# Optimization experiments

Hardware: AMD Instinct MI355X
Metric: run time of the kernel (lower is better)

The kernel has to match this reference:

```python
import jax, jax.numpy as jnp
import numpy as np

HYP_C = 0.1
TAU = 0.1
MRG = 0.1
CLIP_R = 2.3
BS = 1024
NB_PROXIES = 256
SZ_EMBED = 128
T_BATCH = BS * 50
T_LCA = NB_PROXIES * 50


@jax.custom_vjp
def artanh(x):
    xc = jnp.clip(x, -1.0 + 1e-5, 1.0 - 1e-5)
    return 0.5 * (jnp.log1p(xc) - jnp.log1p(-xc))

def _artanh_fwd(x):
    xc = jnp.clip(x, -1.0 + 1e-5, 1.0 - 1e-5)
    return 0.5 * (jnp.log1p(xc) - jnp.log1p(-xc)), xc

def _artanh_bwd(xc, g):
    return (g / (1.0 - xc * xc),)

artanh.defvjp(_artanh_fwd, _artanh_bwd)


@jax.custom_vjp
def riemannian_fix(x):
    # identity fwd; bwd rescales euclidean grad to riemannian grad on the ball
    return x

def _riem_fwd(x):
    return x, x

def _riem_bwd(x, g):
    scale = ((1.0 - HYP_C * jnp.sum(x * x, axis=-1, keepdims=True)) ** 2) / 4.0
    return (g * scale,)

riemannian_fix.defvjp(_riem_fwd, _riem_bwd)


def expmap0(x, c):
    sqrt_c = c ** 0.5
    xn = jnp.maximum(jnp.linalg.norm(x, axis=-1, keepdims=True), 1e-5)
    return jnp.tanh(sqrt_c * xn) * x / (sqrt_c * xn)


def project(x, c):
    norm = jnp.maximum(jnp.linalg.norm(x, axis=-1, keepdims=True), 1e-5)
    maxnorm = (1.0 - 1e-3) / (c ** 0.5)
    return jnp.where(norm > maxnorm, x / norm * maxnorm, x)


def to_poincare(x, c, clip_r):
    xn = jnp.linalg.norm(x, axis=-1, keepdims=True) + 1e-5
    x = x * jnp.minimum(jnp.ones_like(xn), clip_r / xn)
    return riemannian_fix(project(expmap0(x, c), c))


def dist_matrix(x, y, c):
    # ||mobius_add(-x, y)|| computed in closed form (same math as the [N,M,D]
    # num/denom construction in the torch code; num_{nm} = a*( -x_n ) + b*y_m).
    sqrt_c = c ** 0.5
    xy = -jnp.einsum('nd,md->nm', x, y)        # (-x) . y
    x2 = jnp.sum(x * x, axis=-1, keepdims=True)  # [N,1]
    y2t = jnp.sum(y * y, axis=-1)[None, :]       # [1,M]
    a = 1.0 + 2.0 * c * xy + c * y2t             # coeff of -x
    b = 1.0 - c * x2                             # coeff of y
    denom = 1.0 + 2.0 * c * xy + (c ** 2) * x2 * y2t
    num_sq = a * a * x2 + 2.0 * a * b * xy + b * b * y2t
    norm = jnp.sqrt(jnp.maximum(num_sq, 1e-12)) / jnp.abs(denom + 1e-5)
    return (2.0 / sqrt_c) * artanh(sqrt_c * norm)


def gumbel_softmax_hard(logits, g):
    # straight-through hard gumbel softmax (tau=1 as in F.gumbel_softmax default)
    y = jax.nn.softmax(logits + g, axis=-1)
    hard = jax.nn.one_hot(jnp.argmax(y, axis=-1), y.shape[-1], dtype=y.dtype)
    return y + jax.lax.stop_gradient(hard - y)


def compute_ghhc(cp_dist, trip, g):
    i, j, k = trip[0], trip[1], trip[2]
    di, dj, dk = cp_dist[i], cp_dist[j], cp_dist[k]   # [T,P] each
    max_ij = jnp.maximum(di, dj)
    p_ij = gumbel_softmax_hard(-max_ij / TAU, g[0])
    max_ijk = jnp.maximum(dk, max_ij)
    p_ijk = gumbel_softmax_hard(-max_ijk / TAU, g[1])
    diff_lca = (jnp.argmax(p_ij, -1) != jnp.argmax(p_ijk, -1)).astype(cp_dist.dtype)
    d_i_ij = jnp.sum(di * p_ij, axis=1)
    d_i_ijk = jnp.sum(di * p_ijk, axis=1)
    d_j_ij = jnp.sum(dj * p_ij, axis=1)
    d_j_ijk = jnp.sum(dj * p_ijk, axis=1)
    d_k_ij = jnp.sum(dk * p_ij, axis=1)
    d_k_ijk = jnp.sum(dk * p_ijk, axis=1)
    hc = (jax.nn.relu(d_i_ij - d_i_ijk + MRG)
          + jax.nn.relu(d_j_ij - d_j_ijk + MRG)
          + jax.nn.relu(d_k_ijk - d_k_ij + MRG))
    return jnp.mean(hc * diff_lca)


def hp_loss(z_s, t_s, lcas, trip1, trip2, trip3, trip4, g1, g2, g3, g4):
    bs = z_s.shape[0]
    lh = to_poincare(lcas, HYP_C, CLIP_R)
    all_nodes = jnp.concatenate([z_s, lh], axis=0)
    D = dist_matrix(all_nodes, all_nodes, HYP_C)
    t_all = jnp.concatenate([t_s, lh], axis=0)
    Dt = dist_matrix(t_all, t_all, HYP_C)
    loss = compute_ghhc(D[:bs, bs:], trip1, g1)
    loss = loss + compute_ghhc(D[bs:, bs:], trip2, g2)
    loss = loss + compute_ghhc(Dt[:bs, bs:], trip3, g3)
    loss = loss + compute_ghhc(Dt[bs:, bs:], trip4, g4)
    return loss


def setup_inputs() -> dict:
    key = jax.random.key(0)
    ks = jax.random.split(key, 12)
    z_s = jax.random.normal(ks[0], (BS, SZ_EMBED), dtype=jnp.float32)
    t_s = jax.random.normal(ks[1], (BS, SZ_EMBED), dtype=jnp.float32)
    y = jax.random.uniform(ks[2], (BS, 24), dtype=jnp.float32)
    # lcas param init: randn / sqrt(d) * clip_r * 0.9
    lcas = jax.random.normal(ks[3], (NB_PROXIES, SZ_EMBED), dtype=jnp.float32)
    lcas = lcas / np.sqrt(SZ_EMBED) * CLIP_R * 0.9
    trip1 = jax.random.randint(ks[4], (3, T_BATCH), 0, BS, dtype=jnp.int32)
    trip2 = jax.random.randint(ks[5], (3, T_LCA), 0, NB_PROXIES, dtype=jnp.int32)
    trip3 = jax.random.randint(ks[6], (3, T_BATCH), 0, BS, dtype=jnp.int32)
    trip4 = jax.random.randint(ks[7], (3, T_LCA), 0, NB_PROXIES, dtype=jnp.int32)
    g1 = jax.random.gumbel(ks[8], (2, T_BATCH, NB_PROXIES), dtype=jnp.float32)
    g2 = jax.random.gumbel(ks[9], (2, T_LCA, NB_PROXIES), dtype=jnp.float32)
    g3 = jax.random.gumbel(ks[10], (2, T_BATCH, NB_PROXIES), dtype=jnp.float32)
    g4 = jax.random.gumbel(ks[11], (2, T_LCA, NB_PROXIES), dtype=jnp.float32)
    return {"z_s": z_s, "t_s": t_s, "y": y, "lcas": lcas,
            "trip1": trip1, "trip2": trip2, "trip3": trip3, "trip4": trip4,
            "g1": g1, "g2": g2, "g3": g3, "g4": g4}


def reference(z_s, t_s, y, lcas, trip1, trip2, trip3, trip4, g1, g2, g3, g4):
    # y only feeds the detached numpy mining loop in the original; the mined
    # triplets are supplied precomputed (trip1..4), so y does not enter the math.
    return hp_loss(z_s, t_s, lcas, trip1, trip2, trip3, trip4, g1, g2, g3, g4)
```

## Files before the change

kernel.cpp:

```cpp
#include <hip/hip_runtime.h>
#include <cstddef>
#include <stdint.h>

#define HYP_C   0.1f
#define SQRT_C  0.31622776601683794f
#define CLIP_R  2.3f
#define MRG     0.1f
#define NPROX   256
#define DIM     128

#define OFF_LH   0
#define OFF_LHT  32768
#define OFF_LN2  65536
#define OFF_D1   65792
#define OFF_D2   327936
#define OFF_D3   393472

__global__ __launch_bounds__(128)
void to_poincare_kernel(const float* __restrict__ lcas,
                        float* __restrict__ ws,
                        float* __restrict__ out)
{
    const int row = blockIdx.x;
    const int k   = threadIdx.x;
    if (row == 0 && k == 0) out[0] = 0.0f;

    float v  = lcas[row * DIM + k];
    float ss = v * v;
    #pragma unroll
    for (int off = 32; off >= 1; off >>= 1)
        ss += __shfl_xor(ss, off, 64);
    __shared__ float wpart[2];
    if ((k & 63) == 0) wpart[k >> 6] = ss;
    __syncthreads();
    const float sumsq = wpart[0] + wpart[1];

    const float s1 = sqrtf(sumsq);
    const float xn = s1 + 1e-5f;
    const float f1 = fminf(1.0f, CLIP_R / xn);
    const float xn2 = fmaxf(f1 * s1, 1e-5f);
    const float th  = tanhf(SQRT_C * xn2);
    const float f2  = th / (SQRT_C * xn2);
    const float nr      = fmaxf(f2 * f1 * s1, 1e-5f);
    const float maxnorm = (1.0f - 1e-3f) / SQRT_C;
    const float f3      = (nr > maxnorm) ? (maxnorm / nr) : 1.0f;

    const float f  = f3 * f2 * f1;
    const float lv = f * v;
    ws[OFF_LH  + row * DIM + k]   = lv;
    ws[OFF_LHT + k * NPROX + row] = lv;
    if (k == 0) ws[OFF_LN2 + row] = f * f * sumsq;
}

__global__ __launch_bounds__(256)
void dist_all_kernel(const float* __restrict__ z,
                     const float* __restrict__ t,
                     float* __restrict__ ws, int nb1)
{
    const float* lhT = ws + OFF_LHT;
    const float* ln2 = ws + OFF_LN2;

    int b = blockIdx.x;
    const float* X; float* Dout; int row0;
    if (b < nb1)            { X = z;            Dout = ws + OFF_D1; row0 = b * 4; }
    else if (b < nb1 + 64)  { X = ws + OFF_LH;  Dout = ws + OFF_D2; row0 = (b - nb1) * 4; }
    else                    { X = t;            Dout = ws + OFF_D3; row0 = (b - nb1 - 64) * 4; }

    __shared__ float xs[4][DIM];
    __shared__ float sx2[4];

    for (int idx = threadIdx.x; idx < 4 * DIM; idx += 256)
        xs[idx / DIM][idx % DIM] = X[row0 * DIM + idx];
    __syncthreads();

    const int wid  = threadIdx.x >> 6;
    const int lane = threadIdx.x & 63;
    {
        float a = xs[wid][lane];
        float c = xs[wid][lane + 64];
        float s = a * a + c * c;
        #pragma unroll
        for (int off = 32; off >= 1; off >>= 1)
            s += __shfl_xor(s, off, 64);
        if (lane == 0) sx2[wid] = s;
    }
    __syncthreads();

    const int m = threadIdx.x;
    float dot0 = 0.f, dot1 = 0.f, dot2 = 0.f, dot3 = 0.f;
    #pragma unroll 8
    for (int k = 0; k < DIM; k += 4) {
        const float4 x0 = *(const float4*)&xs[0][k];
        const float4 x1 = *(const float4*)&xs[1][k];
        const float4 x2 = *(const float4*)&xs[2][k];
        const float4 x3 = *(const float4*)&xs[3][k];
        const float l0 = lhT[(k + 0) * NPROX + m];
        const float l1 = lhT[(k + 1) * NPROX + m];
        const float l2 = lhT[(k + 2) * NPROX + m];
        const float l3 = lhT[(k + 3) * NPROX + m];
        dot0 = fmaf(x0.x, l0, fmaf(x0.y, l1, fmaf(x0.z, l2, fmaf(x0.w, l3, dot0))));
        dot1 = fmaf(x1.x, l0, fmaf(x1.y, l1, fmaf(x1.z, l2, fmaf(x1.w, l3, dot1))));
        dot2 = fmaf(x2.x, l0, fmaf(x2.y, l1, fmaf(x2.z, l2, fmaf(x2.w, l3, dot2))));
        dot3 = fmaf(x3.x, l0, fmaf(x3.y, l1, fmaf(x3.z, l2, fmaf(x3.w, l3, dot3))));
    }

    const float y2 = ln2[m];
    float dots[4] = {dot0, dot1, dot2, dot3};
    #pragma unroll
    for (int r = 0; r < 4; ++r) {
        const float x2 = sx2[r];
        const float xy = -dots[r];
        const float a  = 1.0f + 2.0f * HYP_C * xy + HYP_C * y2;
        const float bb = 1.0f - HYP_C * x2;
        const float denom  = 1.0f + 2.0f * HYP_C * xy + HYP_C * HYP_C * x2 * y2;
        const float num_sq = a * a * x2 + 2.0f * a * bb * xy + bb * bb * y2;
        const float nrm = sqrtf(fmaxf(num_sq, 1e-12f)) / fabsf(denom + 1e-5f);
        float u = SQRT_C * nrm;
        u = fminf(fmaxf(u, -1.0f + 1e-5f), 1.0f - 1e-5f);
        const float d = (2.0f / SQRT_C) * (0.5f * (log1pf(u) - log1pf(-u)));
        Dout[(size_t)(row0 + r) * NPROX + m] = d;
    }
}

__device__ __forceinline__ float dpp_fmax16(float x) {
    int o;
    o = __builtin_amdgcn_update_dpp(0, __float_as_int(x), 0x121, 0xF, 0xF, true);
    x = fmaxf(x, __int_as_float(o));
    o = __builtin_amdgcn_update_dpp(0, __float_as_int(x), 0x122, 0xF, 0xF, true);
    x = fmaxf(x, __int_as_float(o));
    o = __builtin_amdgcn_update_dpp(0, __float_as_int(x), 0x124, 0xF, 0xF, true);
    x = fmaxf(x, __int_as_float(o));
    o = __builtin_amdgcn_update_dpp(0, __float_as_int(x), 0x128, 0xF, 0xF, true);
    x = fmaxf(x, __int_as_float(o));
    return x;
}

__device__ __forceinline__ int dpp_imin16(int x) {
    int o;
    o = __builtin_amdgcn_update_dpp(0, x, 0x121, 0xF, 0xF, true); x = min(x, o);
    o = __builtin_amdgcn_update_dpp(0, x, 0x122, 0xF, 0xF, true); x = min(x, o);
    o = __builtin_amdgcn_update_dpp(0, x, 0x124, 0xF, 0xF, true); x = min(x, o);
    o = __builtin_amdgcn_update_dpp(0, x, 0x128, 0xF, 0xF, true); x = min(x, o);
    return x;
}

__device__ __forceinline__ float wave_fmax(float x) {
    x = dpp_fmax16(x);
    x = fmaxf(x, __shfl_xor(x, 16, 64));
    x = fmaxf(x, __shfl_xor(x, 32, 64));
    return x;
}

__device__ __forceinline__ int wave_imin(int x) {
    x = dpp_imin16(x);
    x = min(x, __shfl_xor(x, 16, 64));
    x = min(x, __shfl_xor(x, 32, 64));
    return x;
}

__global__ __launch_bounds__(256)
void ghhc_fused_kernel(const float* __restrict__ Da, const float* __restrict__ Db,
                       const float* __restrict__ Dc, const float* __restrict__ Dd,
                       const int* __restrict__ ta, const int* __restrict__ tb,
                       const int* __restrict__ tc, const int* __restrict__ td,
                       const float* __restrict__ ga, const float* __restrict__ gb,
                       const float* __restrict__ gc, const float* __restrict__ gd,
                       int Ta, int Tb, int Tc, int Td,
                       float sa, float sb, float sc_, float sd,
                       int nba, int nbb, int nbc,
                       float* __restrict__ out)
{
    const int tid  = threadIdx.x;
    const int w    = tid >> 6;
    const int lane = tid & 63;

    const int b = blockIdx.x;
    const float* D; const int* tr; const float* g; int Tt; float sc; int lb;
    if (b < nba)                   { D = Da; tr = ta; g = ga; Tt = Ta; sc = sa;  lb = b; }
    else if (b < nba + nbb)        { D = Db; tr = tb; g = gb; Tt = Tb; sc = sb;  lb = b - nba; }
    else if (b < nba + nbb + nbc)  { D = Dc; tr = tc; g = gc; Tt = Tc; sc = sc_; lb = b - nba - nbb; }
    else                           { D = Dd; tr = td; g = gd; Tt = Td; sc = sd;  lb = b - nba - nbb - nbc; }

    const int tstart = lb * 64 + w * 16;

    int tl = tstart + (lane & 15);
    tl = (tl < Tt) ? tl : (Tt - 1);
    const int idxi = tr[tl];
    const int idxj = tr[Tt + tl];
    const int idxk = tr[2 * Tt + tl];

    float4 bdi[3], bdj[3], bdk[3], bg0[3], bg1[3];

    #define ISSUE(IT) { \
        const int t_  = tstart + (IT); \
        const int te_ = (t_ < Tt) ? t_ : (Tt - 1); \
        const int i_  = __shfl(idxi, (IT) & 15, 64); \
        const int j_  = __shfl(idxj, (IT) & 15, 64); \
        const int k_  = __shfl(idxk, (IT) & 15, 64); \
        bdi[(IT) % 3] = ((const float4*)(D + (size_t)i_ * NPROX))[lane]; \
        bdj[(IT) % 3] = ((const float4*)(D + (size_t)j_ * NPROX))[lane]; \
        bdk[(IT) % 3] = ((const float4*)(D + (size_t)k_ * NPROX))[lane]; \
        bg0[(IT) % 3] = ((const float4*)(g + (size_t)te_ * NPROX))[lane]; \
        bg1[(IT) % 3] = ((const float4*)(g + ((size_t)Tt + te_) * NPROX))[lane]; \
    }

    float acc = 0.0f;
    float pdiA = 0.f, pdjA = 0.f, pdkA = 0.f, pdiB = 0.f, pdjB = 0.f, pdkB = 0.f;
    bool  pC = false;

    ISSUE(0); ISSUE(1); ISSUE(2);

    #define STEP(IT) { \
        const float4 di = bdi[(IT) % 3]; \
        const float4 dj = bdj[(IT) % 3]; \
        const float4 dk = bdk[(IT) % 3]; \
        const float4 q0 = bg0[(IT) % 3]; \
        const float4 q1 = bg1[(IT) % 3]; \
        float S0, S1, S2, S3, U0, U1, U2, U3; \
        { float m1, m2; \
          m1 = fmaxf(di.x, dj.x); S0 = fmaf(m1, -10.0f, q0.x); m2 = fmaxf(dk.x, m1); U0 = fmaf(m2, -10.0f, q1.x); \
          m1 = fmaxf(di.y, dj.y); S1 = fmaf(m1, -10.0f, q0.y); m2 = fmaxf(dk.y, m1); U1 = fmaf(m2, -10.0f, q1.y); \
          m1 = fmaxf(di.z, dj.z); S2 = fmaf(m1, -10.0f, q0.z); m2 = fmaxf(dk.z, m1); U2 = fmaf(m2, -10.0f, q1.z); \
          m1 = fmaxf(di.w, dj.w); S3 = fmaf(m1, -10.0f, q0.w); m2 = fmaxf(dk.w, m1); U3 = fmaf(m2, -10.0f, q1.w); } \
        if ((IT) + 3 < 16) ISSUE((IT) + 3) \
        const float gvA = wave_fmax(fmaxf(fmaxf(S0, S1), fmaxf(S2, S3))); \
        const float gvB = wave_fmax(fmaxf(fmaxf(U0, U1), fmaxf(U2, U3))); \
        int slA = 4, slB = 4; \
        slA = (S3 == gvA) ? 3 : slA; slA = (S2 == gvA) ? 2 : slA; \
        slA = (S1 == gvA) ? 1 : slA; slA = (S0 == gvA) ? 0 : slA; \
        slB = (U3 == gvB) ? 3 : slB; slB = (U2 == gvB) ? 2 : slB; \
        slB = (U1 == gvB) ? 1 : slB; slB = (U0 == gvB) ? 0 : slB; \
        const int eA = (slA < 4) ? ((lane << 2) | slA) : 1024; \
        const int eB = (slB < 4) ? ((lane << 2) | slB) : 1024; \
        const int Ag = wave_imin(eA); \
        const int Bg = wave_imin(eB); \
        const int i_ = __shfl(idxi, (IT) & 15, 64); \
        const int j_ = __shfl(idxj, (IT) & 15, 64); \
        const int k_ = __shfl(idxk, (IT) & 15, 64); \
        const float* Ri = D + (size_t)i_ * NPROX; \
        const float* Rj = D + (size_t)j_ * NPROX; \
        const float* Rk = D + (size_t)k_ * NPROX; \
        const float nDiA = Ri[Ag], nDiB = Ri[Bg]; \
        const float nDjA = Rj[Ag], nDjB = Rj[Bg]; \
        const float nDkA = Rk[Ag], nDkB = Rk[Bg]; \
        if ((IT) > 0) { \
            const float hc = fmaxf(pdiA - pdiB + MRG, 0.0f) \
                           + fmaxf(pdjA - pdjB + MRG, 0.0f) \
                           + fmaxf(pdkB - pdkA + MRG, 0.0f); \
            acc += (pC && lane == 0) ? hc * sc : 0.0f; \
        } \
        pdiA = nDiA; pdiB = nDiB; pdjA = nDjA; pdjB = nDjB; pdkA = nDkA; pdkB = nDkB; \
        pC = ((tstart + (IT)) < Tt) && (Ag != Bg); \
    }

    STEP(0)  STEP(1)  STEP(2)  STEP(3)
    STEP(4)  STEP(5)  STEP(6)  STEP(7)
    STEP(8)  STEP(9)  STEP(10) STEP(11)
    STEP(12) STEP(13) STEP(14) STEP(15)

    #undef STEP
    #undef ISSUE

    {
        const float hc = fmaxf(pdiA - pdiB + MRG, 0.0f)
                       + fmaxf(pdjA - pdjB + MRG, 0.0f)
                       + fmaxf(pdkB - pdkA + MRG, 0.0f);
        acc += (pC && lane == 0) ? hc * sc : 0.0f;
    }

    __shared__ float wsum[4];
    if (lane == 0) wsum[w] = acc;
    __syncthreads();
    if (tid == 0)
        atomicAdd(out, wsum[0] + wsum[1] + wsum[2] + wsum[3]);
}

extern "C" void kernel_launch(void* const* d_in, const int* in_sizes, int n_in,
                              void* d_out, int out_size, void* d_ws, size_t ws_size,
                              hipStream_t stream)
{
    const float* z_s  = (const float*)d_in[0];
    const float* t_s  = (const float*)d_in[1];
    const float* lcas = (const float*)d_in[3];
    const int* trip1 = (const int*)d_in[4];
    const int* trip2 = (const int*)d_in[5];
    const int* trip3 = (const int*)d_in[6];
    const int* trip4 = (const int*)d_in[7];
    const float* g1 = (const float*)d_in[8];
    const float* g2 = (const float*)d_in[9];
    const float* g3 = (const float*)d_in[10];
    const float* g4 = (const float*)d_in[11];
    float* out = (float*)d_out;
    float* ws  = (float*)d_ws;

    const int T1 = in_sizes[4] / 3;
    const int T2 = in_sizes[5] / 3;
    const int T3 = in_sizes[6] / 3;
    const int T4 = in_sizes[7] / 3;
    const int BS = in_sizes[0] / DIM;
    const int nb1 = BS / 4;

    to_poincare_kernel<<<NPROX, 128, 0, stream>>>(lcas, ws, out);

    dist_all_kernel<<<2 * nb1 + 64, 256, 0, stream>>>(z_s, t_s, ws, nb1);

    const int nbA = (T1 + 63) / 64;
    const int nbB = (T2 + 63) / 64;
    const int nbC = (T3 + 63) / 64;
    const int nbD = (T4 + 63) / 64;
    ghhc_fused_kernel<<<nbA + nbB + nbC + nbD, 256, 0, stream>>>(
        ws + OFF_D1, ws + OFF_D2, ws + OFF_D3, ws + OFF_D2,
        trip1, trip2, trip3, trip4,
        g1, g2, g3, g4,
        T1, T2, T3, T4,
        1.0f / (float)T1, 1.0f / (float)T2, 1.0f / (float)T3, 1.0f / (float)T4,
        nbA, nbB, nbC,
        out);
}
```

Measured before the change: 307.3 us.

## Stream gathered rows into LDS asynchronously and shuffle selected distances

Replaces the register triple-buffered float4 row loads with a per-wave LDS double buffer filled by async global_load_lds, using explicit vmcnt waits and sched barriers. The six dependent per-step scalar global loads that fetched the distances at the two argmax positions are dropped. Those values are now taken from registers already holding the rows, via lane select and wave shuffles. This removes the deferred-accumulation pipeline. It adds LDS pressure and hand-tuned wait counts, and the prefetch distance drops from three steps to two.

```diff
diff --git a/kernel.cpp b/kernel.cpp
--- a/kernel.cpp
+++ b/kernel.cpp
@@ -158,6 +158,20 @@
     return x;
 }
 
+__device__ __forceinline__ void ld_row_async(const float* src, const float* lds_dst, int lane) {
+    typedef __attribute__((address_space(3))) uint32_t as3_u32;
+    typedef const __attribute__((address_space(1))) uint32_t as1_u32;
+    __builtin_amdgcn_global_load_lds((as1_u32*)(src + 4 * lane),
+                                     (as3_u32*)(uint32_t)(uintptr_t)lds_dst,
+                                     16, 0, 0);
+}
+
+__device__ __forceinline__ float sel4(const float4 v, int c) {
+    const float lo = (c & 1) ? v.y : v.x;
+    const float hi = (c & 1) ? v.w : v.z;
+    return (c & 2) ? hi : lo;
+}
+
 __global__ __launch_bounds__(256)
 void ghhc_fused_kernel(const float* __restrict__ Da, const float* __restrict__ Db,
                        const float* __restrict__ Dc, const float* __restrict__ Dd,
@@ -189,7 +203,8 @@
     const int idxj = tr[Tt + tl];
     const int idxk = tr[2 * Tt + tl];
 
-    float4 bdi[3], bdj[3], bdk[3], bg0[3], bg1[3];
+    __shared__ float sbuf[4 * 2 * 5 * 256];
+    float* const wbase = sbuf + w * 2560;
 
     #define ISSUE(IT) { \
         const int t_  = tstart + (IT); \
@@ -197,32 +212,36 @@
         const int i_  = __shfl(idxi, (IT) & 15, 64); \
         const int j_  = __shfl(idxj, (IT) & 15, 64); \
         const int k_  = __shfl(idxk, (IT) & 15, 64); \
-        bdi[(IT) % 3] = ((const float4*)(D + (size_t)i_ * NPROX))[lane]; \
-        bdj[(IT) % 3] = ((const float4*)(D + (size_t)j_ * NPROX))[lane]; \
-        bdk[(IT) % 3] = ((const float4*)(D + (size_t)k_ * NPROX))[lane]; \
-        bg0[(IT) % 3] = ((const float4*)(g + (size_t)te_ * NPROX))[lane]; \
-        bg1[(IT) % 3] = ((const float4*)(g + ((size_t)Tt + te_) * NPROX))[lane]; \
+        float* B_ = wbase + ((IT) & 1) * 1280; \
+        ld_row_async(D + (size_t)i_ * NPROX,          B_ +    0, lane); \
+        ld_row_async(D + (size_t)j_ * NPROX,          B_ +  256, lane); \
+        ld_row_async(D + (size_t)k_ * NPROX,          B_ +  512, lane); \
+        ld_row_async(g + (size_t)te_ * NPROX,         B_ +  768, lane); \
+        ld_row_async(g + ((size_t)Tt + te_) * NPROX,  B_ + 1024, lane); \
     }
 
     float acc = 0.0f;
-    float pdiA = 0.f, pdjA = 0.f, pdkA = 0.f, pdiB = 0.f, pdjB = 0.f, pdkB = 0.f;
-    bool  pC = false;
-
-    ISSUE(0); ISSUE(1); ISSUE(2);
+
+    ISSUE(0); ISSUE(1);
 
     #define STEP(IT) { \
-        const float4 di = bdi[(IT) % 3]; \
-        const float4 dj = bdj[(IT) % 3]; \
-        const float4 dk = bdk[(IT) % 3]; \
-        const float4 q0 = bg0[(IT) % 3]; \
-        const float4 q1 = bg1[(IT) % 3]; \
+        if ((IT) == 15) { asm volatile("s_waitcnt vmcnt(0)" ::: "memory"); } \
+        else            { asm volatile("s_waitcnt vmcnt(5)" ::: "memory"); } \
+        __builtin_amdgcn_sched_barrier(0); \
+        const float* B_ = wbase + ((IT) & 1) * 1280; \
+        const float4 di = ((const float4*)(B_ +    0))[lane]; \
+        const float4 dj = ((const float4*)(B_ +  256))[lane]; \
+        const float4 dk = ((const float4*)(B_ +  512))[lane]; \
+        const float4 q0 = ((const float4*)(B_ +  768))[lane]; \
+        const float4 q1 = ((const float4*)(B_ + 1024))[lane]; \
         float S0, S1, S2, S3, U0, U1, U2, U3; \
         { float m1, m2; \
           m1 = fmaxf(di.x, dj.x); S0 = fmaf(m1, -10.0f, q0.x); m2 = fmaxf(dk.x, m1); U0 = fmaf(m2, -10.0f, q1.x); \
           m1 = fmaxf(di.y, dj.y); S1 = fmaf(m1, -10.0f, q0.y); m2 = fmaxf(dk.y, m1); U1 = fmaf(m2, -10.0f, q1.y); \
           m1 = fmaxf(di.z, dj.z); S2 = fmaf(m1, -10.0f, q0.z); m2 = fmaxf(dk.z, m1); U2 = fmaf(m2, -10.0f, q1.z); \
           m1 = fmaxf(di.w, dj.w); S3 = fmaf(m1, -10.0f, q0.w); m2 = fmaxf(dk.w, m1); U3 = fmaf(m2, -10.0f, q1.w); } \
-        if ((IT) + 3 < 16) ISSUE((IT) + 3) \
+        __builtin_amdgcn_sched_barrier(0); \
+        if ((IT) + 2 < 16) ISSUE((IT) + 2) \
         const float gvA = wave_fmax(fmaxf(fmaxf(S0, S1), fmaxf(S2, S3))); \
         const float gvB = wave_fmax(fmaxf(fmaxf(U0, U1), fmaxf(U2, U3))); \
         int slA = 4, slB = 4; \
@@ -234,23 +253,18 @@
         const int eB = (slB < 4) ? ((lane << 2) | slB) : 1024; \
         const int Ag = wave_imin(eA); \
         const int Bg = wave_imin(eB); \
-        const int i_ = __shfl(idxi, (IT) & 15, 64); \
-        const int j_ = __shfl(idxj, (IT) & 15, 64); \
-        const int k_ = __shfl(idxk, (IT) & 15, 64); \
-        const float* Ri = D + (size_t)i_ * NPROX; \
-        const float* Rj = D + (size_t)j_ * NPROX; \
-        const float* Rk = D + (size_t)k_ * NPROX; \
-        const float nDiA = Ri[Ag], nDiB = Ri[Bg]; \
-        const float nDjA = Rj[Ag], nDjB = Rj[Bg]; \
-        const float nDkA = Rk[Ag], nDkB = Rk[Bg]; \
-        if ((IT) > 0) { \
-            const float hc = fmaxf(pdiA - pdiB + MRG, 0.0f) \
-                           + fmaxf(pdjA - pdjB + MRG, 0.0f) \
-                           + fmaxf(pdkB - pdkA + MRG, 0.0f); \
-            acc += (pC && lane == 0) ? hc * sc : 0.0f; \
-        } \
-        pdiA = nDiA; pdiB = nDiB; pdjA = nDjA; pdjB = nDjB; pdkA = nDkA; pdkB = nDkB; \
-        pC = ((tstart + (IT)) < Tt) && (Ag != Bg); \
+        const int lA = Ag >> 2, cA = Ag & 3; \
+        const int lB = Bg >> 2, cB = Bg & 3; \
+        const float diA = __shfl(sel4(di, cA), lA, 64); \
+        const float djA = __shfl(sel4(dj, cA), lA, 64); \
+        const float dkA = __shfl(sel4(dk, cA), lA, 64); \
+        const float diB = __shfl(sel4(di, cB), lB, 64); \
+        const float djB = __shfl(sel4(dj, cB), lB, 64); \
+        const float dkB = __shfl(sel4(dk, cB), lB, 64); \
+        const float hc = fmaxf(diA - diB + MRG, 0.0f) \
+                       + fmaxf(djA - djB + MRG, 0.0f) \
+                       + fmaxf(dkB - dkA + MRG, 0.0f); \
+        acc += (((tstart + (IT)) < Tt) && (Ag != Bg) && lane == 0) ? hc * sc : 0.0f; \
     }
 
     STEP(0)  STEP(1)  STEP(2)  STEP(3)
@@ -261,18 +275,10 @@
     #undef STEP
     #undef ISSUE
 
-    {
-        const float hc = fmaxf(pdiA - pdiB + MRG, 0.0f)
-                       + fmaxf(pdjA - pdjB + MRG, 0.0f)
-                       + fmaxf(pdkB - pdkA + MRG, 0.0f);
-        acc += (pC && lane == 0) ? hc * sc : 0.0f;
-    }
-
-    __shared__ float wsum[4];
-    if (lane == 0) wsum[w] = acc;
+    if (lane == 0) wbase[0] = acc;
     __syncthreads();
     if (tid == 0)
-        atomicAdd(out, wsum[0] + wsum[1] + wsum[2] + wsum[3]);
+        atomicAdd(out, sbuf[0] + sbuf[2560] + sbuf[5120] + sbuf[7680]);
 }
 
 extern "C" void kernel_launch(void* const* d_in, const int* in_sizes, int n_in,
```

New measurement: 305.1 us. No clear change (-0.7%).
